# Performance work log

Measured on AMD Instinct MI355X. Metric: run time of the kernel, lower is better.

The kernel has to match this reference:

```python
import jax, jax.numpy as jnp
import numpy as np

CODEBOOK_SIZE = 8192
HIDDEN_SIZE = 256
N_ANCHORS = 5


def setup_inputs() -> dict:
    key = jax.random.key(0)
    k1, k2 = jax.random.split(key)
    z = jax.random.normal(k1, (8, 4096, HIDDEN_SIZE), dtype=jnp.float32)
    emb = 0.02 * jax.random.normal(k2, (CODEBOOK_SIZE, HIDDEN_SIZE), dtype=jnp.float32)
    # enforce_anchor_values(): first 5 rows are one-hot anchors (eye padded with zeros)
    anchors = jnp.zeros((N_ANCHORS, HIDDEN_SIZE), dtype=jnp.float32)
    anchors = anchors.at[:, :N_ANCHORS].set(jnp.eye(N_ANCHORS, dtype=jnp.float32))
    emb = emb.at[:N_ANCHORS, :].set(anchors)
    return {"z": z, "emb": emb}


def reference(z, emb):
    b, t, h = z.shape
    flat = z.reshape(b * t, h)
    # squared L2 distance: ||z||^2 - 2 z.e + ||e||^2  -> [b*t, K]
    dist = (
        jnp.sum(flat * flat, axis=1, keepdims=True)
        - 2.0 * (flat @ emb.T)
        + jnp.sum(emb * emb, axis=1)[None, :]
    )
    idx = jnp.argmin(dist, axis=1)  # [b*t]
    z_q = emb[idx].reshape(b, t, h)
    # straight-through estimator
    z_st = z + jax.lax.stop_gradient(z_q - z)
    codebook_loss = jnp.mean((z_q - jax.lax.stop_gradient(z)) ** 2)
    commit_loss = jnp.mean((z - jax.lax.stop_gradient(z_q)) ** 2)
    return z_st, idx.reshape(b, t), codebook_loss, commit_loss
```

## Files before the change

kernel.cpp:

```cpp
#include <hip/hip_runtime.h>

#define HIDDEN 256
#define K_CODES 8192
#define N_TOK 32768
#define ZST_ELEMS 8388608
#define N_ANCHORS 5
#define NCH 64
#define MARGIN 8.0e-3f
#define WLS_CAP 131072
#define WLC_CAP 131072
#define EPI_BLOCKS 8192

using short8 = __attribute__((ext_vector_type(8))) short;
using f32x4  = __attribute__((ext_vector_type(4))) float;

__device__ __forceinline__ unsigned short f2bf(float f) {
    unsigned int u = __float_as_uint(f);
    return (unsigned short)((u + 0x7fffu + ((u >> 16) & 1u)) >> 16);
}

__device__ __forceinline__ void gl2lds16(const void* g, void* l) {
    __builtin_amdgcn_global_load_lds(
        (const __attribute__((address_space(1))) unsigned int*)g,
        (__attribute__((address_space(3))) unsigned int*)l, 16, 0, 0);
}

__device__ __forceinline__ unsigned long long score_key(float s, int code) {
    unsigned int u = __float_as_uint(s);
    u = (u & 0x80000000u) ? ~u : (u | 0x80000000u);
    return (((unsigned long long)u) << 32) | (unsigned int)code;
}

__global__ void prep_kernel(const float* __restrict__ emb, const float* __restrict__ z,
                            float* __restrict__ ne, float* __restrict__ zn,
                            unsigned short* __restrict__ Bh, unsigned short* __restrict__ Ah) {
#pragma clang fp contract(off)
    int gt  = blockIdx.x * 256 + threadIdx.x;
    int row = gt >> 4;
    int sub = gt & 15;
    const float* src; unsigned short* dst; float* nrm;
    if (row < K_CODES) {
        src = emb + (size_t)row * HIDDEN;
        dst = Bh  + (size_t)row * HIDDEN;
        nrm = ne + row;
    } else {
        int r2 = row - K_CODES;
        src = z  + (size_t)r2 * HIDDEN;
        dst = Ah + (size_t)r2 * HIDDEN;
        nrm = zn + r2;
    }
    const float* p = src + (sub >> 3) * 128 + (sub & 7);
    float v = p[0];
    float r = v * v;
    #pragma unroll
    for (int i = 1; i < 16; ++i) { float w = p[8 * i]; r += w * w; }
    r += __shfl_xor(r, 1, 64);
    r += __shfl_xor(r, 2, 64);
    r += __shfl_xor(r, 4, 64);
    r += __shfl_xor(r, 8, 64);
    if (sub == 0) *nrm = r;

    const float4* s4 = (const float4*)src + sub * 4;
    #pragma unroll
    for (int j = 0; j < 2; ++j) {
        float4 a = s4[2 * j];
        float4 b = s4[2 * j + 1];
        short8 h;
        h[0] = (short)f2bf(a.x); h[1] = (short)f2bf(a.y);
        h[2] = (short)f2bf(a.z); h[3] = (short)f2bf(a.w);
        h[4] = (short)f2bf(b.x); h[5] = (short)f2bf(b.y);
        h[6] = (short)f2bf(b.z); h[7] = (short)f2bf(b.w);
        *(short8*)(dst + sub * 16 + j * 8) = h;
    }
}

__global__ __launch_bounds__(512, 4) void mfma_score_kernel(
    const unsigned short* __restrict__ Ah,
    const unsigned short* __restrict__ Bh,
    const float* __restrict__ ne,
    float* __restrict__ p1, float* __restrict__ p2, unsigned short* __restrict__ piu) {

    __shared__ unsigned short Ahs[2][256 * 32];
    __shared__ unsigned short Bhs[2][128 * 32];

    const int tid  = threadIdx.x;
    const int wm   = tid >> 6;
    const int lane = tid & 63;
    const int L    = lane & 15;
    const int q    = lane >> 4;

    const int lin  = blockIdx.x;
    const int xcd  = lin & 7;
    const int s    = lin >> 3;
    const int nb   = s >> 4;
    const int m0   = (xcd * 16 + (s & 15)) * 256;
    const int n0   = nb * 128;

    f32x4 acc[2][8] = {};

    auto STAGE = [&](int kt, int buf) {
        const int k0 = kt * 32;
        #pragma unroll
        for (int r = 0; r < 2; ++r) {
            int u   = tid + 512 * r;
            int row = u >> 2;
            int p   = u & 3;
            int ch  = p ^ ((row >> 1) & 3);
            gl2lds16(Ah + (size_t)(m0 + row) * HIDDEN + k0 + ch * 8,
                     &Ahs[buf][u * 8]);
        }
        {
            int u   = tid;
            int row = u >> 2;
            int p   = u & 3;
            int ch  = p ^ ((row >> 1) & 3);
            gl2lds16(Bh + (size_t)(n0 + row) * HIDDEN + k0 + ch * 8,
                     &Bhs[buf][u * 8]);
        }
    };

    STAGE(0, 0);
    STAGE(1, 1);
    asm volatile("s_waitcnt vmcnt(3)" ::: "memory");
    __builtin_amdgcn_s_barrier();
    asm volatile("" ::: "memory");

    #pragma unroll
    for (int kt = 0; kt < 8; ++kt) {
        const int cur = kt & 1;

        const short8* A8h = (const short8*)Ahs[cur];
        const short8* B8h = (const short8*)Bhs[cur];

        short8 ah[2];
        #pragma unroll
        for (int tm = 0; tm < 2; ++tm) {
            int m  = wm * 32 + tm * 16 + L;
            ah[tm] = A8h[m * 4 + (q ^ ((m >> 1) & 3))];
        }
        #pragma unroll
        for (int tn = 0; tn < 8; ++tn) {
            int n  = tn * 16 + L;
            short8 bh = B8h[n * 4 + (q ^ ((n >> 1) & 3))];
            #pragma unroll
            for (int tm = 0; tm < 2; ++tm) {
                acc[tm][tn] = __builtin_amdgcn_mfma_f32_16x16x32_bf16(
                    ah[tm], bh, acc[tm][tn], 0, 0, 0);
            }
        }

        if (kt < 7) {
            __builtin_amdgcn_s_barrier();
            asm volatile("" ::: "memory");
            if (kt + 2 < 8) {
                STAGE(kt + 2, cur);
                asm volatile("s_waitcnt vmcnt(3)" ::: "memory");
            } else {
                asm volatile("s_waitcnt vmcnt(0)" ::: "memory");
            }
            __builtin_amdgcn_s_barrier();
            asm volatile("" ::: "memory");
        }
    }

    float nev[8];
    #pragma unroll
    for (int tn = 0; tn < 8; ++tn) nev[tn] = ne[n0 + tn * 16 + L];
    if (nb == 0 && L < N_ANCHORS) nev[0] = 3.4e38f;

    #pragma unroll
    for (int tm = 0; tm < 2; ++tm) {
        #pragma unroll
        for (int reg = 0; reg < 4; ++reg) {
            float m1 = 3.4e38f, m2 = 3.4e38f;
            int bi = 0;
            #pragma unroll
            for (int tn = 0; tn < 8; ++tn) {
                float s2 = nev[tn] - 2.0f * acc[tm][tn][reg];
                int lo = tn * 16 + L;
                if (s2 < m1)      { m2 = m1; m1 = s2; bi = lo; }
                else if (s2 < m2) { m2 = s2; }
            }
            #pragma unroll
            for (int off = 1; off < 16; off <<= 1) {
                float o1 = __shfl_xor(m1, off, 64);
                float o2 = __shfl_xor(m2, off, 64);
                int   oi = __shfl_xor(bi, off, 64);
                if (o1 < m1 || (o1 == m1 && oi < bi)) {
                    m2 = fminf(m1, o2); m1 = o1; bi = oi;
                } else {
                    m2 = fminf(m2, o1);
                }
            }
            if (L == 0) {
                size_t mrow = (size_t)m0 + wm * 32 + tm * 16 + q * 4 + reg;
                p1[(size_t)nb * N_TOK + mrow]  = m1;
                p2[(size_t)nb * N_TOK + mrow]  = m2;
                piu[(size_t)nb * N_TOK + mrow] = (unsigned short)bi;
            }
        }
    }
}

__global__ void combine_kernel(const float* __restrict__ p1, const float* __restrict__ p2,
                               const unsigned short* __restrict__ piu,
                               const float* __restrict__ z, const float* __restrict__ zn,
                               const float* __restrict__ ne,
                               float* __restrict__ idxf, int* __restrict__ flags,
                               unsigned long long* __restrict__ slots,
                               int* __restrict__ wls, int* __restrict__ wlc,
                               unsigned int* __restrict__ wcnt) {
#pragma clang fp contract(off)
    int t = blockIdx.x * 256 + threadIdx.x;
    float m1 = 3.4e38f, m2 = 3.4e38f;
    int bi = 0;
    for (int nb = 0; nb < NCH; ++nb) {
        float o1 = p1[(size_t)nb * N_TOK + t];
        float o2 = p2[(size_t)nb * N_TOK + t];
        if (o1 < m1) {
            m2 = fminf(m1, o2); m1 = o1;
            bi = nb * 128 + (int)piu[(size_t)nb * N_TOK + t];
        } else {
            m2 = fminf(m2, o1);
        }
    }
    float zt = zn[t];
    const float* zp = z + (size_t)t * HIDDEN;
    float sa = 3.4e38f; int ai = 0;
    #pragma unroll
    for (int a = 0; a < N_ANCHORS; ++a) {
        float s = (zt - 2.0f * zp[a]) + ne[a];
        if (s < sa) { sa = s; ai = a; }
    }
    slots[t] = score_key(sa, ai);
    float g = sa - zt;
    bool anchorWin = (g + MARGIN < m1);
    bool amb = !anchorWin && ((m2 - m1 < MARGIN) || (g <= m1 + MARGIN));
    idxf[t]  = anchorWin ? (float)ai : (float)bi;
    flags[t] = amb ? 1 : 0;
    if (amb) {
        float thr = m1 + MARGIN;
        for (int nb = 0; nb < NCH; ++nb) {
            float o1 = p1[(size_t)nb * N_TOK + t];
            if (o1 <= thr) {
                if (p2[(size_t)nb * N_TOK + t] <= thr) {
                    unsigned int pos = atomicAdd(&wcnt[1], 2u);
                    if (pos + 1 < WLC_CAP) {
                        wlc[pos]     = (t << 7) | (nb * 2);
                        wlc[pos + 1] = (t << 7) | (nb * 2 + 1);
                    }
                } else {
                    unsigned int pos = atomicAdd(&wcnt[0], 1u);
                    if (pos < WLS_CAP)
                        wls[pos] = (t << 13) | (nb * 128 + (int)piu[(size_t)nb * N_TOK + t]);
                }
            }
        }
    }
}

__global__ __launch_bounds__(256) void rescue_fused(
    const float* __restrict__ z, const float* __restrict__ emb,
    const float* __restrict__ ne, const float* __restrict__ zn,
    const int* __restrict__ wls, const int* __restrict__ wlc,
    const unsigned int* __restrict__ wcnt,
    unsigned long long* __restrict__ slots) {
#pragma clang fp contract(off)
    int ns = (int)wcnt[0];
    if (ns > WLS_CAP) ns = WLS_CAP;
    for (int i = blockIdx.x * 256 + threadIdx.x; i < ns; i += gridDim.x * 256) {
        int it = wls[i];
        int t  = it >> 13;
        int c  = it & (K_CODES - 1);
        const float4* zp = (const float4*)(z + (size_t)t * HIDDEN);
        const float4* ep = (const float4*)(emb + (size_t)c * HIDDEN);
        float acc = 0.0f;
        #pragma unroll 8
        for (int k4 = 0; k4 < 64; ++k4) {
            float4 zv = zp[k4];
            float4 ev = ep[k4];
            acc = __builtin_fmaf(ev.x, zv.x, acc);
            acc = __builtin_fmaf(ev.y, zv.y, acc);
            acc = __builtin_fmaf(ev.z, zv.z, acc);
            acc = __builtin_fmaf(ev.w, zv.w, acc);
        }
        float s = (zn[t] - 2.0f * acc) + ne[c];
        atomicMin(&slots[t], score_key(s, c));
    }

    int nit = (int)wcnt[1];
    if (nit > WLC_CAP) nit = WLC_CAP;
    const int lane = threadIdx.x & 63;
    const int wid  = (blockIdx.x * 256 + threadIdx.x) >> 6;
    const int nw   = gridDim.x * 4;

    for (int item = wid; item < nit; item += nw) {
        int w   = wlc[item];
        int t   = w >> 7;
        int nb2 = w & 127;
        int c   = nb2 * 64 + lane;
        const float4* e4  = (const float4*)(emb + (size_t)c * HIDDEN);
        const float4* zp4 = (const float4*)(z + (size_t)t * HIDDEN);
        float acc = 0.0f;
        #pragma unroll 8
        for (int k4 = 0; k4 < 64; ++k4) {
            float4 zv = zp4[k4];
            float4 ev = e4[k4];
            acc = __builtin_fmaf(ev.x, zv.x, acc);
            acc = __builtin_fmaf(ev.y, zv.y, acc);
            acc = __builtin_fmaf(ev.z, zv.z, acc);
            acc = __builtin_fmaf(ev.w, zv.w, acc);
        }
        float t1 = zn[t] - 2.0f * acc;
        float s  = t1 + ne[c];

        unsigned long long key = score_key(s, c);
        #pragma unroll
        for (int off = 1; off < 64; off <<= 1) {
            unsigned long long o = __shfl_xor(key, off, 64);
            if (o < key) key = o;
        }
        if (lane == 0) atomicMin(&slots[t], key);
    }
}

__global__ void epilogue_kernel(const float* __restrict__ z, const float* __restrict__ emb,
                                const int* __restrict__ flags,
                                const unsigned long long* __restrict__ slots,
                                float* __restrict__ idxf, float* __restrict__ zst,
                                float* __restrict__ loss_part) {
    int t4    = blockIdx.x * 256 + threadIdx.x;
    int token = t4 >> 6;
    int k4    = t4 & 63;

    int idx;
    if (flags[token]) idx = (int)(unsigned int)(slots[token] & 0xFFFFFFFFULL);
    else              idx = (int)idxf[token];
    if (k4 == 0) idxf[token] = (float)idx;

    float4 zv = ((const float4*)z)[t4];
    float4 ev = ((const float4*)emb)[(size_t)idx * 64 + k4];

    float dx = ev.x - zv.x, dy = ev.y - zv.y, dz = ev.z - zv.z, dw = ev.w - zv.w;
    float4 o = { zv.x + dx, zv.y + dy, zv.z + dz, zv.w + dw };
    ((float4*)zst)[t4] = o;

    float p = dx * dx + dy * dy + dz * dz + dw * dw;
    #pragma unroll
    for (int off = 32; off; off >>= 1) p += __shfl_down(p, off, 64);

    __shared__ float wsum[4];
    int lane = threadIdx.x & 63, w = threadIdx.x >> 6;
    if (lane == 0) wsum[w] = p;
    __syncthreads();
    if (threadIdx.x == 0)
        loss_part[blockIdx.x] = wsum[0] + wsum[1] + wsum[2] + wsum[3];
}

__global__ __launch_bounds__(256) void finalize_kernel(
    const float* __restrict__ loss_part, float* __restrict__ out_losses) {
    float s = 0.0f;
    for (int i = threadIdx.x; i < EPI_BLOCKS; i += 256) s += loss_part[i];
    #pragma unroll
    for (int off = 32; off; off >>= 1) s += __shfl_down(s, off, 64);
    __shared__ float ws[4];
    int lane = threadIdx.x & 63, w = threadIdx.x >> 6;
    if (lane == 0) ws[w] = s;
    __syncthreads();
    if (threadIdx.x == 0) {
        float m = (ws[0] + ws[1] + ws[2] + ws[3]) * (1.0f / (float)ZST_ELEMS);
        out_losses[0] = m;
        out_losses[1] = m;
    }
}

extern "C" void kernel_launch(void* const* d_in, const int* in_sizes, int n_in,
                              void* d_out, int out_size, void* d_ws, size_t ws_size,
                              hipStream_t stream) {
    const float* z   = (const float*)d_in[0];
    const float* emb = (const float*)d_in[1];

    float* out    = (float*)d_out;
    float* zst    = out;
    float* idxf   = out + ZST_ELEMS;
    float* losses = out + ZST_ELEMS + N_TOK;

    char* w = (char*)d_ws;
    unsigned short* Ah = (unsigned short*)w;    w += (size_t)N_TOK  * HIDDEN * 2;
    unsigned short* Bh = (unsigned short*)w;    w += (size_t)K_CODES * HIDDEN * 2;
    float* p1 = (float*)w;                      w += (size_t)NCH * N_TOK * 4;
    float* p2 = (float*)w;                      w += (size_t)NCH * N_TOK * 4;
    unsigned short* piu = (unsigned short*)w;   w += (size_t)NCH * N_TOK * 2;
    float* ne = (float*)w;                      w += K_CODES * 4;
    float* zn = (float*)w;                      w += N_TOK * 4;
    int*   flags = (int*)w;                     w += N_TOK * 4;
    unsigned long long* slots = (unsigned long long*)w;  w += N_TOK * 8;
    int*   wls = (int*)w;                       w += (size_t)WLS_CAP * 4;
    int*   wlc = (int*)w;                       w += (size_t)WLC_CAP * 4;
    float* loss_part = (float*)w;               w += (size_t)EPI_BLOCKS * 4;
    unsigned int* wcnt = (unsigned int*)w;

    hipMemsetAsync(wcnt, 0, 8, stream);
    prep_kernel<<<(K_CODES + N_TOK) * 16 / 256, 256, 0, stream>>>(emb, z, ne, zn, Bh, Ah);
    mfma_score_kernel<<<N_TOK / 256 * NCH, 512, 0, stream>>>(Ah, Bh, ne, p1, p2, piu);
    combine_kernel<<<N_TOK / 256, 256, 0, stream>>>(p1, p2, piu, z, zn, ne,
                                                    idxf, flags, slots, wls, wlc, wcnt);
    rescue_fused<<<1024, 256, 0, stream>>>(z, emb, ne, zn, wls, wlc, wcnt, slots);
    epilogue_kernel<<<EPI_BLOCKS, 256, 0, stream>>>(z, emb, flags, slots,
                                                    idxf, zst, loss_part);
    finalize_kernel<<<1, 256, 0, stream>>>(loss_part, losses);
}
```

Measured before the change: 436.4 us.

## Split combine across 8 lanes per token and simplify GEMM double-buffer sync

The combine kernel now assigns eight threads per token, each scanning eight of the 64 chunk partials, then merges (min1, min2, index) with xor shuffles. Per-chunk values are kept in registers for the ambiguous-candidate pass instead of being re-read. Only sub-lane 0 writes the per-token outputs. Separately, the MFMA score kernel's two-stage prefetch with explicit vmcnt waits is replaced by a simpler prefetch-next-tile plus __syncthreads per k-step, which may lower how much load latency is hidden.

```diff
diff --git a/kernel.cpp b/kernel.cpp
--- a/kernel.cpp
+++ b/kernel.cpp
@@ -120,14 +120,12 @@
     };
 
     STAGE(0, 0);
-    STAGE(1, 1);
-    asm volatile("s_waitcnt vmcnt(3)" ::: "memory");
-    __builtin_amdgcn_s_barrier();
-    asm volatile("" ::: "memory");
+    __syncthreads();
 
     #pragma unroll
     for (int kt = 0; kt < 8; ++kt) {
         const int cur = kt & 1;
+        if (kt < 7) STAGE(kt + 1, cur ^ 1);
 
         const short8* A8h = (const short8*)Ahs[cur];
         const short8* B8h = (const short8*)Bhs[cur];
@@ -148,19 +146,7 @@
                     ah[tm], bh, acc[tm][tn], 0, 0, 0);
             }
         }
-
-        if (kt < 7) {
-            __builtin_amdgcn_s_barrier();
-            asm volatile("" ::: "memory");
-            if (kt + 2 < 8) {
-                STAGE(kt + 2, cur);
-                asm volatile("s_waitcnt vmcnt(3)" ::: "memory");
-            } else {
-                asm volatile("s_waitcnt vmcnt(0)" ::: "memory");
-            }
-            __builtin_amdgcn_s_barrier();
-            asm volatile("" ::: "memory");
-        }
+        if (kt < 7) __syncthreads();
     }
 
     float nev[8];
@@ -211,12 +197,19 @@
                                int* __restrict__ wls, int* __restrict__ wlc,
                                unsigned int* __restrict__ wcnt) {
 #pragma clang fp contract(off)
-    int t = blockIdx.x * 256 + threadIdx.x;
+    int gt  = blockIdx.x * 256 + threadIdx.x;
+    int t   = gt >> 3;
+    int sub = gt & 7;
+
+    float o1v[8], o2v[8];
     float m1 = 3.4e38f, m2 = 3.4e38f;
     int bi = 0;
-    for (int nb = 0; nb < NCH; ++nb) {
+    #pragma unroll
+    for (int j = 0; j < 8; ++j) {
+        int nb = sub + j * 8;
         float o1 = p1[(size_t)nb * N_TOK + t];
         float o2 = p2[(size_t)nb * N_TOK + t];
+        o1v[j] = o1; o2v[j] = o2;
         if (o1 < m1) {
             m2 = fminf(m1, o2); m1 = o1;
             bi = nb * 128 + (int)piu[(size_t)nb * N_TOK + t];
@@ -224,6 +217,17 @@
             m2 = fminf(m2, o1);
         }
     }
+    #pragma unroll
+    for (int off = 1; off < 8; off <<= 1) {
+        float o1 = __shfl_xor(m1, off, 64);
+        float o2 = __shfl_xor(m2, off, 64);
+        int   oi = __shfl_xor(bi, off, 64);
+        if (o1 < m1 || (o1 == m1 && oi < bi)) {
+            m2 = fminf(m1, o2); m1 = o1; bi = oi;
+        } else {
+            m2 = fminf(m2, o1);
+        }
+    }
     float zt = zn[t];
     const float* zp = z + (size_t)t * HIDDEN;
     float sa = 3.4e38f; int ai = 0;
@@ -232,18 +236,21 @@
         float s = (zt - 2.0f * zp[a]) + ne[a];
         if (s < sa) { sa = s; ai = a; }
     }
-    slots[t] = score_key(sa, ai);
     float g = sa - zt;
     bool anchorWin = (g + MARGIN < m1);
     bool amb = !anchorWin && ((m2 - m1 < MARGIN) || (g <= m1 + MARGIN));
-    idxf[t]  = anchorWin ? (float)ai : (float)bi;
-    flags[t] = amb ? 1 : 0;
+    if (sub == 0) {
+        slots[t] = score_key(sa, ai);
+        idxf[t]  = anchorWin ? (float)ai : (float)bi;
+        flags[t] = amb ? 1 : 0;
+    }
     if (amb) {
         float thr = m1 + MARGIN;
-        for (int nb = 0; nb < NCH; ++nb) {
-            float o1 = p1[(size_t)nb * N_TOK + t];
-            if (o1 <= thr) {
-                if (p2[(size_t)nb * N_TOK + t] <= thr) {
+        #pragma unroll
+        for (int j = 0; j < 8; ++j) {
+            int nb = sub + j * 8;
+            if (o1v[j] <= thr) {
+                if (o2v[j] <= thr) {
                     unsigned int pos = atomicAdd(&wcnt[1], 2u);
                     if (pos + 1 < WLC_CAP) {
                         wlc[pos]     = (t << 7) | (nb * 2);
@@ -403,8 +410,8 @@
     hipMemsetAsync(wcnt, 0, 8, stream);
     prep_kernel<<<(K_CODES + N_TOK) * 16 / 256, 256, 0, stream>>>(emb, z, ne, zn, Bh, Ah);
     mfma_score_kernel<<<N_TOK / 256 * NCH, 512, 0, stream>>>(Ah, Bh, ne, p1, p2, piu);
-    combine_kernel<<<N_TOK / 256, 256, 0, stream>>>(p1, p2, piu, z, zn, ne,
-                                                    idxf, flags, slots, wls, wlc, wcnt);
+    combine_kernel<<<N_TOK * 8 / 256, 256, 0, stream>>>(p1, p2, piu, z, zn, ne,
+                                                        idxf, flags, slots, wls, wlc, wcnt);
     rescue_fused<<<1024, 256, 0, stream>>>(z, emb, ne, zn, wls, wlc, wcnt, slots);
     epilogue_kernel<<<EPI_BLOCKS, 256, 0, stream>>>(z, emb, flags, slots,
                                                     idxf, zst, loss_part);
```

After: 414.8 us. 4.9% less time.
